# Kernel optimization log

Measured on AMD Instinct MI355X. Metric: run time of the kernel, lower is better.

## Reference

```python
import jax, jax.numpy as jnp
import numpy as np


def setup_inputs() -> dict:
    key = jax.random.key(0)
    k1, k2 = jax.random.split(key)
    B, C, N = 8, 3, 4096
    ori_pcs = jax.random.normal(k1, (B, C, N), dtype=jnp.float32)
    adv_pcs = jax.random.normal(k2, (B, C, N), dtype=jnp.float32)
    return {"ori_pcs": ori_pcs, "adv_pcs": adv_pcs}


def _chamfer(ori_pcs, adv_pcs, single=False, reduce="max"):
    # [B, 3, N] -> [B, N, 3]
    x = jnp.swapaxes(ori_pcs, 1, 2)
    y = jnp.swapaxes(adv_pcs, 1, 2)
    x2 = jnp.sum(x * x, axis=-1)  # [B, N]
    y2 = jnp.sum(y * y, axis=-1)  # [B, M]
    # squared pairwise distances [B, N, M]
    d = x2[:, :, None] + y2[:, None, :] - 2.0 * jnp.einsum("bnd,bmd->bnm", x, y)
    d = jnp.maximum(d, 0.0)
    d1 = jnp.mean(jnp.min(d, axis=2), axis=1)  # ori -> adv, per batch [B]
    if single:
        return jnp.mean(d1)
    d2 = jnp.mean(jnp.min(d, axis=1), axis=1)  # adv -> ori, per batch [B]
    if reduce == "max":
        per_batch = jnp.maximum(d1, d2)
    else:  # 'sum' / 'mean' style fallback
        per_batch = d1 + d2
    return jnp.mean(per_batch)


def reference(ori_pcs, adv_pcs):
    return _chamfer(ori_pcs, adv_pcs, single=False, reduce="max")
```

## Files before the change

kernel.cpp:

```cpp
#include <hip/hip_runtime.h>
#include <float.h>

#define BATCH 8
#define NPTS 4096
#define BLK 512
#define THALF 1024
#define NH 4

typedef __attribute__((ext_vector_type(8))) short short8;
typedef __attribute__((ext_vector_type(16))) float floatx16;

union U4S8 { uint4 u; short8 s; };

__device__ inline unsigned short f2bf(float f) {
    unsigned u = __float_as_uint(f);
    return (unsigned short)((u + 0x7FFFu + ((u >> 16) & 1u)) >> 16);
}
__device__ inline float bf2f(unsigned short h) {
    return __uint_as_float(((unsigned)h) << 16);
}
__device__ inline unsigned flag_token(int i) {
    return 0x9E3779B9u * (unsigned)(i + 7);
}

__global__ __launch_bounds__(BLK, 4) void chamfer_partial(
        const float* __restrict__ ori, const float* __restrict__ adv,
        float* __restrict__ rfin) {
    __shared__ uint4 sm[THALF];

    int bx = blockIdx.x;
    int half = bx & (NH - 1);
    int rowgroup = (bx >> 2) & 15;
    int dirb = bx >> 6;
    int b = dirb & 7;
    int dir = dirb >> 3;

    const float* qsrc = dir ? adv : ori;
    const float* tsrc = dir ? ori : adv;

    {
        const float* tx = tsrc + (b * 3 + 0) * NPTS;
        const float* ty = tsrc + (b * 3 + 1) * NPTS;
        const float* tz = tsrc + (b * 3 + 2) * NPTS;
        #pragma unroll
        for (int i = 0; i < THALF / BLK; ++i) {
            int p = threadIdx.x + i * BLK;
            int m = half * THALF + p;
            float x = tx[m], y = ty[m], z = tz[m];
            float n2 = fmaf(x, x, fmaf(y, y, z * z));
            unsigned short hx = f2bf(x), hy = f2bf(y), hz = f2bf(z);
            unsigned short lx = f2bf(x - bf2f(hx));
            unsigned short ly = f2bf(y - bf2f(hy));
            unsigned short lz = f2bf(z - bf2f(hz));
            unsigned short h2 = f2bf(n2);
            unsigned short l2 = f2bf(n2 - bf2f(h2));
            uint4 u;
            u.x = (unsigned)hx | ((unsigned)hy << 16);
            u.y = (unsigned)hz | ((unsigned)lx << 16);
            u.z = (unsigned)ly | ((unsigned)lz << 16);
            u.w = (unsigned)h2 | ((unsigned)l2 << 16);
            sm[p] = u;
        }
    }

    int w = threadIdx.x >> 6;
    int l = threadIdx.x & 63;
    int lrow = l & 31;
    int kh = l >> 5;

    short8 afrag;
    {
        int q = rowgroup * 256 + w * 32 + lrow;
        float x = qsrc[(b * 3 + 0) * NPTS + q];
        float y = qsrc[(b * 3 + 1) * NPTS + q];
        float z = qsrc[(b * 3 + 2) * NPTS + q];
        float n2 = fmaf(x, x, fmaf(y, y, z * z));
        unsigned short hx = f2bf(x), hy = f2bf(y), hz = f2bf(z);
        unsigned short lx = f2bf(x - bf2f(hx));
        unsigned short ly = f2bf(y - bf2f(hy));
        unsigned short lz = f2bf(z - bf2f(hz));
        unsigned short h2 = f2bf(n2);
        unsigned short l2 = f2bf(n2 - bf2f(h2));
        unsigned short mhx = f2bf(-2.0f * bf2f(hx));
        unsigned short mhy = f2bf(-2.0f * bf2f(hy));
        unsigned short mhz = f2bf(-2.0f * bf2f(hz));
        unsigned short mlx = f2bf(-2.0f * bf2f(lx));
        unsigned short mly = f2bf(-2.0f * bf2f(ly));
        unsigned short mlz = f2bf(-2.0f * bf2f(lz));
        const unsigned short one = 0x3F80;
        union { unsigned short us[8]; short8 s8; } A;
        if (kh == 0) {
            A.us[0] = mhx; A.us[1] = mhy; A.us[2] = mhz;
            A.us[3] = mhx; A.us[4] = mhy; A.us[5] = mhz;
            A.us[6] = one; A.us[7] = one;
        } else {
            A.us[0] = mlx; A.us[1] = mly; A.us[2] = mlz;
            A.us[3] = h2;  A.us[4] = l2;
            A.us[5] = 0;   A.us[6] = 0;   A.us[7] = 0;
        }
        afrag = A.s8;
    }
    __syncthreads();

    floatx16 zero, rmn;
    #pragma unroll
    for (int r = 0; r < 16; ++r) { zero[r] = 0.0f; rmn[r] = FLT_MAX; }

    bool hi = (kh == 1);
    int col = lrow;

#define PROCESS2(r0, r1)                                                       \
    {                                                                          \
        U4S8 f0, f1;                                                           \
        f0.u.x = (r0).x;                                                       \
        f0.u.y = hi ? (((r0).y & 0xFFFFu) | 0x3F800000u) : (r0).y;             \
        f0.u.z = hi ? 0x00003F80u : (r0).z;                                    \
        f0.u.w = hi ? 0u : (r0).w;                                             \
        f1.u.x = (r1).x;                                                       \
        f1.u.y = hi ? (((r1).y & 0xFFFFu) | 0x3F800000u) : (r1).y;             \
        f1.u.z = hi ? 0x00003F80u : (r1).z;                                    \
        f1.u.w = hi ? 0u : (r1).w;                                             \
        floatx16 a0 = __builtin_amdgcn_mfma_f32_32x32x16_bf16(afrag, f0.s, zero, 0, 0, 0); \
        floatx16 a1 = __builtin_amdgcn_mfma_f32_32x32x16_bf16(afrag, f1.s, zero, 0, 0, 0); \
        _Pragma("unroll")                                                      \
        for (int r = 0; r < 16; ++r)                                           \
            rmn[r] = fminf(fminf(rmn[r], a0[r]), a1[r]);        \
    }

    {
        uint4 r0 = sm[col], r1 = sm[32 + col];
        #pragma unroll 1
        for (int ct = 0; ct < 30; ct += 2) {
            uint4 p0 = sm[(ct + 2) * 32 + col];
            uint4 p1 = sm[(ct + 3) * 32 + col];
            PROCESS2(r0, r1);
            r0 = p0; r1 = p1;
        }
        PROCESS2(r0, r1);
    }
#undef PROCESS2

    #pragma unroll
    for (int r = 0; r < 16; ++r) {
        float v = rmn[r];
        #pragma unroll
        for (int m = 1; m <= 16; m <<= 1)
            v = fminf(v, __shfl_xor(v, m));
        rmn[r] = v;
    }
    if (lrow == 0) {
        float* d = rfin + (((size_t)(dirb * NH + half)) << 12)
                 + rowgroup * 256 + w * 32 + kh * 4;
        #pragma unroll
        for (int r = 0; r < 16; ++r)
            d[(r & 3) + 8 * (r >> 2)] = rmn[r];
    }
}

__global__ __launch_bounds__(256) void combine_kernel(
        const float* __restrict__ rfin, float* __restrict__ bsum,
        unsigned* __restrict__ flags, float* __restrict__ out) {
    __shared__ float ws[4];
    __shared__ float sh[16];
    int dirb = blockIdx.x;
    const float* p = rfin + (((size_t)dirb * NH) << 12);
    float s = 0.0f;
    #pragma unroll
    for (int k = 0; k < 16; ++k) {
        int row = k * 256 + threadIdx.x;
        float m = fminf(fminf(p[row], p[(1 << 12) + row]),
                        fminf(p[(2 << 12) + row], p[(3 << 12) + row]));
        s += fmaxf(m, 0.0f);
    }
    for (int off = 32; off > 0; off >>= 1) s += __shfl_down(s, off);
    int wid = threadIdx.x >> 6, lane = threadIdx.x & 63;
    if (lane == 0) ws[wid] = s;
    __syncthreads();
    if (threadIdx.x == 0) {
        float t = ws[0] + ws[1] + ws[2] + ws[3];
        atomicExch((unsigned*)(bsum + dirb), __float_as_uint(t));
        __threadfence();
        atomicExch(flags + dirb, flag_token(dirb));
    }

    if (dirb == 0) {
        __syncthreads();
        int t = threadIdx.x;
        if (t < 16) {
            unsigned want = flag_token(t);
            while (atomicAdd(flags + t, 0u) != want) {
                __builtin_amdgcn_s_sleep(1);
            }
            sh[t] = __uint_as_float(atomicAdd((unsigned*)(bsum + t), 0u));
        }
        __syncthreads();
        if (t == 0) {
            float acc = 0.0f;
            #pragma unroll
            for (int bb = 0; bb < BATCH; ++bb)
                acc += fmaxf(sh[bb], sh[8 + bb]);
            out[0] = acc * (1.0f / (float)NPTS) * (1.0f / (float)BATCH);
        }
    }
}

extern "C" void kernel_launch(void* const* d_in, const int* in_sizes, int n_in,
                              void* d_out, int out_size, void* d_ws, size_t ws_size,
                              hipStream_t stream) {
    const float* ori = (const float*)d_in[0];
    const float* adv = (const float*)d_in[1];
    float* out = (float*)d_out;

    float* rfin = (float*)d_ws;
    float* bsum = rfin + (size_t)16 * NH * NPTS;
    unsigned* flags = (unsigned*)(bsum + 16);

    chamfer_partial<<<16 * 16 * NH, BLK, 0, stream>>>(ori, adv, rfin);
    combine_kernel<<<16, 256, 0, stream>>>(rfin, bsum, flags, out);
}
```

Measured before the change: 22.66 us.

## Process two query tiles per wave to reuse LDS target fragments

Each wave now holds two 32-row query A-fragments and runs both against every target B-fragment loaded from LDS. This halves the grid and halves the per-block LDS staging and bf16 split work per query row. The final min reduction is replaced by a transpose-style butterfly fold that needs fewer shuffles. The change adds accumulator register pressure and leaves fewer blocks to hide latency.

Result: faster. 19.47 us, median of 2 (-14.1%).

```diff
diff --git a/kernel.cpp b/kernel.cpp
--- a/kernel.cpp
+++ b/kernel.cpp
@@ -6,6 +6,7 @@
 #define BLK 512
 #define THALF 1024
 #define NH 4
+#define NRG 8
 
 typedef __attribute__((ext_vector_type(8))) short short8;
 typedef __attribute__((ext_vector_type(16))) float floatx16;
@@ -30,8 +31,8 @@
 
     int bx = blockIdx.x;
     int half = bx & (NH - 1);
-    int rowgroup = (bx >> 2) & 15;
-    int dirb = bx >> 6;
+    int rowgroup = (bx >> 2) & (NRG - 1);
+    int dirb = bx >> 5;
     int b = dirb & 7;
     int dir = dirb >> 3;
 
@@ -68,9 +69,10 @@
     int lrow = l & 31;
     int kh = l >> 5;
 
-    short8 afrag;
-    {
-        int q = rowgroup * 256 + w * 32 + lrow;
+    short8 afrag0, afrag1;
+    #pragma unroll
+    for (int bi = 0; bi < 2; ++bi) {
+        int q = rowgroup * 512 + (w * 2 + bi) * 32 + lrow;
         float x = qsrc[(b * 3 + 0) * NPTS + q];
         float y = qsrc[(b * 3 + 1) * NPTS + q];
         float z = qsrc[(b * 3 + 2) * NPTS + q];
@@ -98,62 +100,92 @@
             A.us[3] = h2;  A.us[4] = l2;
             A.us[5] = 0;   A.us[6] = 0;   A.us[7] = 0;
         }
-        afrag = A.s8;
+        if (bi == 0) afrag0 = A.s8; else afrag1 = A.s8;
     }
     __syncthreads();
 
-    floatx16 zero, rmn;
+    floatx16 zero, rmn0, rmn1;
     #pragma unroll
-    for (int r = 0; r < 16; ++r) { zero[r] = 0.0f; rmn[r] = FLT_MAX; }
+    for (int r = 0; r < 16; ++r) { zero[r] = 0.0f; rmn0[r] = FLT_MAX; rmn1[r] = FLT_MAX; }
 
     bool hi = (kh == 1);
     int col = lrow;
-
-#define PROCESS2(r0, r1)                                                       \
-    {                                                                          \
-        U4S8 f0, f1;                                                           \
-        f0.u.x = (r0).x;                                                       \
-        f0.u.y = hi ? (((r0).y & 0xFFFFu) | 0x3F800000u) : (r0).y;             \
-        f0.u.z = hi ? 0x00003F80u : (r0).z;                                    \
-        f0.u.w = hi ? 0u : (r0).w;                                             \
-        f1.u.x = (r1).x;                                                       \
-        f1.u.y = hi ? (((r1).y & 0xFFFFu) | 0x3F800000u) : (r1).y;             \
-        f1.u.z = hi ? 0x00003F80u : (r1).z;                                    \
-        f1.u.w = hi ? 0u : (r1).w;                                             \
-        floatx16 a0 = __builtin_amdgcn_mfma_f32_32x32x16_bf16(afrag, f0.s, zero, 0, 0, 0); \
-        floatx16 a1 = __builtin_amdgcn_mfma_f32_32x32x16_bf16(afrag, f1.s, zero, 0, 0, 0); \
-        _Pragma("unroll")                                                      \
-        for (int r = 0; r < 16; ++r)                                           \
-            rmn[r] = fminf(fminf(rmn[r], a0[r]), a1[r]);        \
-    }
 
     {
         uint4 r0 = sm[col], r1 = sm[32 + col];
         #pragma unroll 1
-        for (int ct = 0; ct < 30; ct += 2) {
-            uint4 p0 = sm[(ct + 2) * 32 + col];
-            uint4 p1 = sm[(ct + 3) * 32 + col];
-            PROCESS2(r0, r1);
-            r0 = p0; r1 = p1;
-        }
-        PROCESS2(r0, r1);
-    }
-#undef PROCESS2
-
-    #pragma unroll
-    for (int r = 0; r < 16; ++r) {
-        float v = rmn[r];
-        #pragma unroll
-        for (int m = 1; m <= 16; m <<= 1)
-            v = fminf(v, __shfl_xor(v, m));
-        rmn[r] = v;
-    }
-    if (lrow == 0) {
-        float* d = rfin + (((size_t)(dirb * NH + half)) << 12)
-                 + rowgroup * 256 + w * 32 + kh * 4;
-        #pragma unroll
-        for (int r = 0; r < 16; ++r)
-            d[(r & 3) + 8 * (r >> 2)] = rmn[r];
+        for (int ct = 0; ct < 32; ct += 2) {
+            U4S8 f0, f1;
+            f0.u.x = r0.x;
+            f0.u.y = hi ? ((r0.y & 0xFFFFu) | 0x3F800000u) : r0.y;
+            f0.u.z = hi ? 0x00003F80u : r0.z;
+            f0.u.w = hi ? 0u : r0.w;
+            f1.u.x = r1.x;
+            f1.u.y = hi ? ((r1.y & 0xFFFFu) | 0x3F800000u) : r1.y;
+            f1.u.z = hi ? 0x00003F80u : r1.z;
+            f1.u.w = hi ? 0u : r1.w;
+            int nt = (ct + 2) & 31;
+            r0 = sm[(nt << 5) + col];
+            r1 = sm[((nt + 1) << 5) + col];
+            {
+                floatx16 a0 = __builtin_amdgcn_mfma_f32_32x32x16_bf16(afrag0, f0.s, zero, 0, 0, 0);
+                floatx16 a1 = __builtin_amdgcn_mfma_f32_32x32x16_bf16(afrag0, f1.s, zero, 0, 0, 0);
+                #pragma unroll
+                for (int r = 0; r < 16; ++r)
+                    rmn0[r] = fminf(fminf(rmn0[r], a0[r]), a1[r]);
+            }
+            {
+                floatx16 c0 = __builtin_amdgcn_mfma_f32_32x32x16_bf16(afrag1, f0.s, zero, 0, 0, 0);
+                floatx16 c1 = __builtin_amdgcn_mfma_f32_32x32x16_bf16(afrag1, f1.s, zero, 0, 0, 0);
+                #pragma unroll
+                for (int r = 0; r < 16; ++r)
+                    rmn1[r] = fminf(fminf(rmn1[r], c0[r]), c1[r]);
+            }
+        }
+    }
+
+    bool b0 = (l & 1), b1 = (l & 2), b2 = (l & 4), b3 = (l & 8);
+
+#define FOLD(v)                                                                \
+    {                                                                          \
+        _Pragma("unroll")                                                      \
+        for (int i = 0; i < 8; ++i) {                                          \
+            float send = b0 ? v[i] : v[i + 8];                                 \
+            float recv = __shfl_xor(send, 1);                                  \
+            v[i] = fminf(b0 ? v[i + 8] : v[i], recv);                          \
+        }                                                                      \
+        _Pragma("unroll")                                                      \
+        for (int i = 0; i < 4; ++i) {                                          \
+            float send = b1 ? v[i] : v[i + 4];                                 \
+            float recv = __shfl_xor(send, 2);                                  \
+            v[i] = fminf(b1 ? v[i + 4] : v[i], recv);                          \
+        }                                                                      \
+        _Pragma("unroll")                                                      \
+        for (int i = 0; i < 2; ++i) {                                          \
+            float send = b2 ? v[i] : v[i + 2];                                 \
+            float recv = __shfl_xor(send, 4);                                  \
+            v[i] = fminf(b2 ? v[i + 2] : v[i], recv);                          \
+        }                                                                      \
+        {                                                                      \
+            float send = b3 ? v[0] : v[1];                                     \
+            float recv = __shfl_xor(send, 8);                                  \
+            v[0] = fminf(b3 ? v[1] : v[0], recv);                              \
+        }                                                                      \
+        v[0] = fminf(v[0], __shfl_xor(v[0], 16));                              \
+    }
+
+    FOLD(rmn0);
+    FOLD(rmn1);
+#undef FOLD
+
+    if ((l & 16) == 0) {
+        int g = l & 15;
+        int rr = ((g & 1) << 3) | ((g & 2) << 1) | ((g & 4) >> 1) | ((g & 8) >> 3);
+        int rowin = (rr & 3) + 8 * (rr >> 2) + 4 * kh;
+        float* base = rfin + (((size_t)(dirb * NH + half)) << 12)
+                    + rowgroup * 512;
+        base[(w * 2 + 0) * 32 + rowin] = rmn0[0];
+        base[(w * 2 + 1) * 32 + rowin] = rmn1[0];
     }
 }
 
@@ -215,6 +247,6 @@
     float* bsum = rfin + (size_t)16 * NH * NPTS;
     unsigned* flags = (unsigned*)(bsum + 16);
 
-    chamfer_partial<<<16 * 16 * NH, BLK, 0, stream>>>(ori, adv, rfin);
+    chamfer_partial<<<16 * NRG * NH, BLK, 0, stream>>>(ori, adv, rfin);
     combine_kernel<<<16, 256, 0, stream>>>(rfin, bsum, flags, out);
 }
```
